# Performance work log

Hardware: AMD Instinct MI355X
Metric: run time of the kernel (lower is better)

Reference implementation:

```python
import jax, jax.numpy as jnp
import numpy as np

N, E, D, ED, G = 100000, 1600000, 64, 64, 512  # nodes, edges, node_dim, edge_dim, graphs
LN_EPS = 1e-5


def setup_inputs() -> dict:
    key = jax.random.key(0)
    ks = jax.random.split(key, 16)
    s_e = 1.0 / np.sqrt(ED)
    s_n = 1.0 / np.sqrt(D)
    inp = {
        'x': jax.random.normal(ks[0], (N, D), jnp.float32),
        'edge_index': jax.random.randint(ks[1], (2, E), 0, N, dtype=jnp.int32),
        'edge_attr': jax.random.normal(ks[2], (E, ED), jnp.float32),
        'node2graph': jnp.sort(jax.random.randint(ks[3], (N,), 0, G, dtype=jnp.int32)),
        # conv1 params
        'We1': jax.random.normal(ks[4], (ED, D), jnp.float32) * s_e,
        'be1': jnp.zeros((D,), jnp.float32),
        'Wm1': jax.random.normal(ks[5], (D, D), jnp.float32) * s_n,
        'bm1': jnp.zeros((D,), jnp.float32),
        'eps1': jnp.array([0.1], jnp.float32),
        'gamma1': jnp.ones((D,), jnp.float32),
        'beta1': jnp.zeros((D,), jnp.float32),
        # conv2 params
        'We2': jax.random.normal(ks[6], (ED, D), jnp.float32) * s_e,
        'be2': jnp.zeros((D,), jnp.float32),
        'Wm2': jax.random.normal(ks[7], (D, D), jnp.float32) * s_n,
        'bm2': jnp.zeros((D,), jnp.float32),
        'eps2': jnp.array([0.1], jnp.float32),
        'gamma2': jnp.ones((D,), jnp.float32),
        'beta2': jnp.zeros((D,), jnp.float32),
    }
    return inp


def _gine_conv(x, src, dst, edge_attr, We, be, Wm, bm, eps):
    # message: SiLU(Wm @ relu(x_j + SiLU(We @ e)) )  gathered per edge, scatter-added to dst
    ea = jax.nn.silu(edge_attr @ We + be)                     # (E, D)
    msg = jax.nn.silu(jnp.maximum(x[src] + ea, 0.0) @ Wm + bm)  # (E, D)
    agg = jax.ops.segment_sum(msg, dst, num_segments=x.shape[0])
    return agg + (1.0 + eps) * x


def _graph_norm(x, g, gamma, beta):
    # pyg LayerNorm(mode='graph'): normalize over all nodes*channels per graph
    f = x.shape[1]
    cnt = jax.ops.segment_sum(jnp.ones((x.shape[0],), x.dtype), g, num_segments=G) * f
    cnt = jnp.maximum(cnt, 1.0)
    mean = jax.ops.segment_sum(x.sum(-1), g, num_segments=G) / cnt          # (G,)
    var = jax.ops.segment_sum((x * x).sum(-1), g, num_segments=G) / cnt - mean ** 2
    xn = (x - mean[g][:, None]) / jnp.sqrt(var + LN_EPS)[g][:, None]
    return xn * gamma + beta


def reference(x, edge_index, edge_attr, node2graph,
              We1, be1, Wm1, bm1, eps1, gamma1, beta1,
              We2, be2, Wm2, bm2, eps2, gamma2, beta2):
    src, dst = edge_index[0], edge_index[1]
    identity = x
    # branch 1 (NOTE: the original torch code computes conv1->norm->relu but then
    # overwrites `out` with conv2(x, ...); we reproduce that faithfully)
    out = _gine_conv(x, src, dst, edge_attr, We1, be1, Wm1, bm1, eps1)
    out = _graph_norm(out, node2graph, gamma1, beta1)
    out = jnp.maximum(out, 0.0)
    # branch 2 (takes original x, per source)
    out = _gine_conv(x, src, dst, edge_attr, We2, be2, Wm2, bm2, eps2)
    out = _graph_norm(out, node2graph, gamma2, beta2)
    out = out + identity
    return jnp.maximum(out, 0.0)
```

## Files before the change

### kernel.cpp

```cpp
#include <hip/hip_runtime.h>
#include <math.h>

#define NN 100000
#define NE 1600000
#define NG 512
#define LN_EPS 1e-5f

typedef __attribute__((ext_vector_type(8))) short short8;
typedef __attribute__((ext_vector_type(8))) unsigned short ushort8;
typedef __attribute__((ext_vector_type(4))) float floatx4;

union BF8 { short8 v; short s[8]; };
union U8  { ushort8 v; unsigned short s[8]; };
union F4  { floatx4 v; float f[4]; };

static __device__ __forceinline__ short f2bf(float f) {
    union { float f; unsigned u; } a; a.f = f;
    unsigned u = a.u;
    unsigned r = (u + 0x7fffu + ((u >> 16) & 1u)) >> 16;
    return (short)r;
}
static __device__ __forceinline__ float bf2f(unsigned short h) {
    union { unsigned u; float f; } a; a.u = ((unsigned)h) << 16;
    return a.f;
}
static __device__ __forceinline__ float silu_f(float v) {
    return v / (1.0f + __expf(-v));
}

__global__ __launch_bounds__(256)
void edge_kernel(const float* __restrict__ x,
                 const int* __restrict__ src,
                 const int* __restrict__ dst,
                 const float* __restrict__ eattr,
                 const float* __restrict__ We,
                 const float* __restrict__ be,
                 const float* __restrict__ Wm,
                 const float* __restrict__ bm,
                 float* __restrict__ agg)
{
    __shared__ unsigned short lds[4][16 * 72];
    const int lane = threadIdx.x & 63;
    const int wid  = threadIdx.x >> 6;
    const int m = lane & 15;
    const int q = lane >> 4;
    unsigned short* tile = lds[wid];

    short8 wef[2][4], wmf[2][4];
    float bev[4], bmv[4];
    #pragma unroll
    for (int kh = 0; kh < 2; ++kh) {
        #pragma unroll
        for (int t = 0; t < 4; ++t) {
            BF8 fe, fm;
            #pragma unroll
            for (int j = 0; j < 8; ++j) {
                const int k = kh * 32 + q * 8 + j;
                const int n = m + 16 * t;
                fe.s[j] = f2bf(We[k * 64 + n]);
                fm.s[j] = f2bf(Wm[k * 64 + n]);
            }
            wef[kh][t] = fe.v; wmf[kh][t] = fm.v;
        }
    }
    #pragma unroll
    for (int t = 0; t < 4; ++t) { bev[t] = be[m + 16 * t]; bmv[t] = bm[m + 16 * t]; }

    const int n_tiles = NE / 16;
    const int stride  = gridDim.x * 4;
    for (int tl = blockIdx.x * 4 + wid; tl < n_tiles; tl += stride) {
        const int e0 = tl * 16;

        short8 a1[2];
        #pragma unroll
        for (int kh = 0; kh < 2; ++kh) {
            const float* p = eattr + (size_t)(e0 + m) * 64 + kh * 32 + q * 8;
            F4 v0, v1; v0.v = *(const floatx4*)p; v1.v = *(const floatx4*)(p + 4);
            BF8 f;
            #pragma unroll
            for (int j = 0; j < 4; ++j) { f.s[j] = f2bf(v0.f[j]); f.s[j + 4] = f2bf(v1.f[j]); }
            a1[kh] = f.v;
        }
        floatx4 acc[4];
        #pragma unroll
        for (int t = 0; t < 4; ++t) acc[t] = (floatx4){0.f, 0.f, 0.f, 0.f};
        #pragma unroll
        for (int kh = 0; kh < 2; ++kh)
            #pragma unroll
            for (int t = 0; t < 4; ++t)
                acc[t] = __builtin_amdgcn_mfma_f32_16x16x32_bf16(a1[kh], wef[kh][t], acc[t], 0, 0, 0);

        #pragma unroll
        for (int t = 0; t < 4; ++t)
            #pragma unroll
            for (int r = 0; r < 4; ++r) {
                const float v = silu_f(acc[t][r] + bev[t]);
                tile[(q * 4 + r) * 72 + m + 16 * t] = (unsigned short)f2bf(v);
            }
        __asm__ volatile("s_waitcnt lgkmcnt(0)" ::: "memory");

        const int sn = src[e0 + m];
        short8 a2[2];
        #pragma unroll
        for (int kh = 0; kh < 2; ++kh) {
            U8 t8; t8.v = *(const ushort8*)&tile[m * 72 + kh * 32 + q * 8];
            const float* xp = x + (size_t)sn * 64 + kh * 32 + q * 8;
            F4 x0, x1; x0.v = *(const floatx4*)xp; x1.v = *(const floatx4*)(xp + 4);
            BF8 f;
            #pragma unroll
            for (int j = 0; j < 4; ++j) {
                f.s[j]     = f2bf(fmaxf(bf2f(t8.s[j])     + x0.f[j], 0.0f));
                f.s[j + 4] = f2bf(fmaxf(bf2f(t8.s[j + 4]) + x1.f[j], 0.0f));
            }
            a2[kh] = f.v;
        }
        #pragma unroll
        for (int t = 0; t < 4; ++t) acc[t] = (floatx4){0.f, 0.f, 0.f, 0.f};
        #pragma unroll
        for (int kh = 0; kh < 2; ++kh)
            #pragma unroll
            for (int t = 0; t < 4; ++t)
                acc[t] = __builtin_amdgcn_mfma_f32_16x16x32_bf16(a2[kh], wmf[kh][t], acc[t], 0, 0, 0);

        int dn[4];
        #pragma unroll
        for (int r = 0; r < 4; ++r) dn[r] = dst[e0 + q * 4 + r];
        #pragma unroll
        for (int t = 0; t < 4; ++t)
            #pragma unroll
            for (int r = 0; r < 4; ++r) {
                const float v = silu_f(acc[t][r] + bmv[t]);
                atomicAdd(agg + (size_t)dn[r] * 64 + (m + 16 * t), v);
            }
    }
}

__global__ __launch_bounds__(256)
void stats_kernel(const float* __restrict__ agg,
                  const float* __restrict__ x,
                  const int* __restrict__ n2g,
                  const float* __restrict__ eps,
                  float* __restrict__ gsum,
                  float* __restrict__ gss,
                  float* __restrict__ gcnt)
{
    const int lane = threadIdx.x & 63;
    const int wid  = threadIdx.x >> 6;
    const float k = 1.0f + eps[0];
    const int stride = gridDim.x * 4;
    for (int n = blockIdx.x * 4 + wid; n < NN; n += stride) {
        const float pre = agg[(size_t)n * 64 + lane] + k * x[(size_t)n * 64 + lane];
        float s = pre, ss = pre * pre;
        #pragma unroll
        for (int off = 32; off > 0; off >>= 1) {
            s  += __shfl_down(s, off, 64);
            ss += __shfl_down(ss, off, 64);
        }
        if (lane == 0) {
            const int g = n2g[n];
            atomicAdd(&gsum[g], s);
            atomicAdd(&gss[g], ss);
            atomicAdd(&gcnt[g], 1.0f);
        }
    }
}

__global__ __launch_bounds__(256)
void norm_kernel(const float* __restrict__ x,
                 const int* __restrict__ n2g,
                 const float* __restrict__ eps,
                 const float* __restrict__ gamma,
                 const float* __restrict__ beta,
                 const float* __restrict__ gsum,
                 const float* __restrict__ gss,
                 const float* __restrict__ gcnt,
                 float* __restrict__ out)
{
    const float k = 1.0f + eps[0];
    const int total = NN * 16;
    for (int idx = blockIdx.x * blockDim.x + threadIdx.x; idx < total;
         idx += gridDim.x * blockDim.x) {
        const int n  = idx >> 4;
        const int c4 = (idx & 15) * 4;
        const int g  = n2g[n];
        const float cnt  = fmaxf(gcnt[g] * 64.0f, 1.0f);
        const float mean = gsum[g] / cnt;
        const float var  = gss[g] / cnt - mean * mean;
        const float rsig = rsqrtf(var + LN_EPS);
        F4 a, xv, o;
        a.v  = *(const floatx4*)&out[(size_t)n * 64 + c4];
        xv.v = *(const floatx4*)&x[(size_t)n * 64 + c4];
        #pragma unroll
        for (int j = 0; j < 4; ++j) {
            const float pre = a.f[j] + k * xv.f[j];
            const float v = (pre - mean) * rsig * gamma[c4 + j] + beta[c4 + j] + xv.f[j];
            o.f[j] = fmaxf(v, 0.0f);
        }
        *(floatx4*)&out[(size_t)n * 64 + c4] = o.v;
    }
}

extern "C" void kernel_launch(void* const* d_in, const int* in_sizes, int n_in,
                              void* d_out, int out_size, void* d_ws, size_t ws_size,
                              hipStream_t stream)
{
    const float* x      = (const float*)d_in[0];
    const int*   ei     = (const int*)  d_in[1];
    const float* eattr  = (const float*)d_in[2];
    const int*   n2g    = (const int*)  d_in[3];
    const float* We2    = (const float*)d_in[11];
    const float* be2    = (const float*)d_in[12];
    const float* Wm2    = (const float*)d_in[13];
    const float* bm2    = (const float*)d_in[14];
    const float* eps2   = (const float*)d_in[15];
    const float* gamma2 = (const float*)d_in[16];
    const float* beta2  = (const float*)d_in[17];

    float* out  = (float*)d_out;
    float* gsum = (float*)d_ws;
    float* gss  = gsum + NG;
    float* gcnt = gss + NG;

    hipMemsetAsync(d_out, 0, (size_t)NN * 64 * sizeof(float), stream);
    hipMemsetAsync(d_ws, 0, 3 * NG * sizeof(float), stream);

    edge_kernel<<<dim3(2048), dim3(256), 0, stream>>>(
        x, ei, ei + NE, eattr, We2, be2, Wm2, bm2, out);
    stats_kernel<<<dim3(1024), dim3(256), 0, stream>>>(
        out, x, n2g, eps2, gsum, gss, gcnt);
    norm_kernel<<<dim3(1024), dim3(256), 0, stream>>>(
        x, n2g, eps2, gamma2, beta2, gsum, gss, gcnt, out);
}
```

Before: 1.064 ms.

## Sort edges by destination and combine duplicate atomics; chunk stats reduction per wave

Builds a destination-sorted permutation of the edges on device each call, using a histogram, a three-kernel scan and an atomic scatter. The edge kernel then processes edges in that order and merges runs of equal destinations within each group of four rows before issuing atomics. The stats kernel now gives each wave a contiguous chunk of nodes and accumulates per graph, flushing only when the graph id changes, which cuts its atomic count. The trade-off is several extra kernel launches and random, uncoalesced gathers of edge_attr through the permutation. With average in-degree 16 and random edges, sorted neighbours in a 16-edge tile will often share a destination.

```diff
diff --git a/kernel.cpp b/kernel.cpp
--- a/kernel.cpp
+++ b/kernel.cpp
@@ -29,10 +29,92 @@
 }
 
 __global__ __launch_bounds__(256)
+void hist_kernel(const int* __restrict__ dst, int* __restrict__ cnt)
+{
+    for (int e = blockIdx.x * blockDim.x + threadIdx.x; e < NE;
+         e += gridDim.x * blockDim.x)
+        atomicAdd(&cnt[dst[e]], 1);
+}
+
+#define SCAN_CHUNK 1024
+#define SCAN_NB ((NN + SCAN_CHUNK - 1) / SCAN_CHUNK)
+
+__global__ __launch_bounds__(256)
+void scan_partial_kernel(const int* __restrict__ cnt, int* __restrict__ bsums)
+{
+    __shared__ int sdata[256];
+    const int b = blockIdx.x, t = threadIdx.x;
+    const int base = b * SCAN_CHUNK + t * 4;
+    int s = 0;
+    #pragma unroll
+    for (int i = 0; i < 4; ++i) {
+        const int idx = base + i;
+        s += (idx < NN) ? cnt[idx] : 0;
+    }
+    sdata[t] = s;
+    __syncthreads();
+    for (int off = 128; off > 0; off >>= 1) {
+        if (t < off) sdata[t] += sdata[t + off];
+        __syncthreads();
+    }
+    if (t == 0) bsums[b] = sdata[0];
+}
+
+__global__ void scan_top_kernel(int* __restrict__ bsums)
+{
+    if (threadIdx.x == 0 && blockIdx.x == 0) {
+        int run = 0;
+        for (int i = 0; i < SCAN_NB; ++i) { const int v = bsums[i]; bsums[i] = run; run += v; }
+    }
+}
+
+__global__ __launch_bounds__(256)
+void scan_final_kernel(int* __restrict__ cnt, const int* __restrict__ bsums)
+{
+    __shared__ int sdata[256];
+    const int b = blockIdx.x, t = threadIdx.x;
+    const int base = b * SCAN_CHUNK + t * 4;
+    int c[4];
+    #pragma unroll
+    for (int i = 0; i < 4; ++i) {
+        const int idx = base + i;
+        c[i] = (idx < NN) ? cnt[idx] : 0;
+    }
+    const int tsum = c[0] + c[1] + c[2] + c[3];
+    sdata[t] = tsum;
+    __syncthreads();
+    for (int off = 1; off < 256; off <<= 1) {
+        const int v = (t >= off) ? sdata[t - off] : 0;
+        __syncthreads();
+        sdata[t] += v;
+        __syncthreads();
+    }
+    int off0 = bsums[b] + sdata[t] - tsum;
+    #pragma unroll
+    for (int i = 0; i < 4; ++i) {
+        const int idx = base + i;
+        if (idx < NN) cnt[idx] = off0;
+        off0 += c[i];
+    }
+}
+
+__global__ __launch_bounds__(256)
+void scatter_kernel(const int* __restrict__ dst, int* __restrict__ starts,
+                    int* __restrict__ perm)
+{
+    for (int e = blockIdx.x * blockDim.x + threadIdx.x; e < NE;
+         e += gridDim.x * blockDim.x) {
+        const int pos = atomicAdd(&starts[dst[e]], 1);
+        perm[pos] = e;
+    }
+}
+
+__global__ __launch_bounds__(256)
 void edge_kernel(const float* __restrict__ x,
                  const int* __restrict__ src,
                  const int* __restrict__ dst,
                  const float* __restrict__ eattr,
+                 const int* __restrict__ perm,
                  const float* __restrict__ We,
                  const float* __restrict__ be,
                  const float* __restrict__ Wm,
@@ -70,11 +152,12 @@
     const int stride  = gridDim.x * 4;
     for (int tl = blockIdx.x * 4 + wid; tl < n_tiles; tl += stride) {
         const int e0 = tl * 16;
+        const int em = perm ? perm[e0 + m] : (e0 + m);
 
         short8 a1[2];
         #pragma unroll
         for (int kh = 0; kh < 2; ++kh) {
-            const float* p = eattr + (size_t)(e0 + m) * 64 + kh * 32 + q * 8;
+            const float* p = eattr + (size_t)em * 64 + kh * 32 + q * 8;
             F4 v0, v1; v0.v = *(const floatx4*)p; v1.v = *(const floatx4*)(p + 4);
             BF8 f;
             #pragma unroll
@@ -99,7 +182,7 @@
             }
         __asm__ volatile("s_waitcnt lgkmcnt(0)" ::: "memory");
 
-        const int sn = src[e0 + m];
+        const int sn = src[em];
         short8 a2[2];
         #pragma unroll
         for (int kh = 0; kh < 2; ++kh) {
@@ -124,17 +207,31 @@
 
         int dn[4];
         #pragma unroll
-        for (int r = 0; r < 4; ++r) dn[r] = dst[e0 + q * 4 + r];
+        for (int r = 0; r < 4; ++r) {
+            const int er = perm ? __shfl(em, q * 4 + r, 64) : (e0 + q * 4 + r);
+            dn[r] = dst[er];
+        }
+        float sv[4][4];
         #pragma unroll
         for (int t = 0; t < 4; ++t)
             #pragma unroll
-            for (int r = 0; r < 4; ++r) {
-                const float v = silu_f(acc[t][r] + bmv[t]);
-                atomicAdd(agg + (size_t)dn[r] * 64 + (m + 16 * t), v);
-            }
-    }
-}
-
+            for (int r = 0; r < 4; ++r)
+                sv[t][r] = silu_f(acc[t][r] + bmv[t]);
+        #pragma unroll
+        for (int t = 0; t < 4; ++t) {
+            const int col = m + 16 * t;
+            float run = sv[t][0];
+            #pragma unroll
+            for (int r = 1; r < 4; ++r) {
+                if (dn[r] == dn[r - 1]) run += sv[t][r];
+                else { atomicAdd(agg + (size_t)dn[r - 1] * 64 + col, run); run = sv[t][r]; }
+            }
+            atomicAdd(agg + (size_t)dn[3] * 64 + col, run);
+        }
+    }
+}
+
+#define STATS_WAVES 4096
 __global__ __launch_bounds__(256)
 void stats_kernel(const float* __restrict__ agg,
                   const float* __restrict__ x,
@@ -146,22 +243,44 @@
 {
     const int lane = threadIdx.x & 63;
     const int wid  = threadIdx.x >> 6;
+    const int w    = blockIdx.x * 4 + wid;
+    const int chunk = (NN + STATS_WAVES - 1) / STATS_WAVES;
+    const int n0 = w * chunk;
+    const int n1 = min(NN, n0 + chunk);
+    if (n0 >= n1) return;
     const float k = 1.0f + eps[0];
-    const int stride = gridDim.x * 4;
-    for (int n = blockIdx.x * 4 + wid; n < NN; n += stride) {
+
+    int   curg = n2g[n0];
+    float s = 0.f, ss = 0.f, rc = 0.f;
+    for (int n = n0; n < n1; ++n) {
+        const int g = n2g[n];
+        if (g != curg) {
+            float a = s, b = ss;
+            #pragma unroll
+            for (int off = 32; off > 0; off >>= 1) {
+                a += __shfl_down(a, off, 64);
+                b += __shfl_down(b, off, 64);
+            }
+            if (lane == 0) {
+                atomicAdd(&gsum[curg], a);
+                atomicAdd(&gss[curg], b);
+                atomicAdd(&gcnt[curg], rc);
+            }
+            s = 0.f; ss = 0.f; rc = 0.f; curg = g;
+        }
         const float pre = agg[(size_t)n * 64 + lane] + k * x[(size_t)n * 64 + lane];
-        float s = pre, ss = pre * pre;
-        #pragma unroll
-        for (int off = 32; off > 0; off >>= 1) {
-            s  += __shfl_down(s, off, 64);
-            ss += __shfl_down(ss, off, 64);
-        }
-        if (lane == 0) {
-            const int g = n2g[n];
-            atomicAdd(&gsum[g], s);
-            atomicAdd(&gss[g], ss);
-            atomicAdd(&gcnt[g], 1.0f);
-        }
+        s += pre; ss += pre * pre; rc += (lane == 0) ? 1.0f : 0.0f;
+    }
+    float a = s, b = ss;
+    #pragma unroll
+    for (int off = 32; off > 0; off >>= 1) {
+        a += __shfl_down(a, off, 64);
+        b += __shfl_down(b, off, 64);
+    }
+    if (lane == 0) {
+        atomicAdd(&gsum[curg], a);
+        atomicAdd(&gss[curg], b);
+        atomicAdd(&gcnt[curg], rc);
     }
 }
 
@@ -215,18 +334,35 @@
     const float* eps2   = (const float*)d_in[15];
     const float* gamma2 = (const float*)d_in[16];
     const float* beta2  = (const float*)d_in[17];
+    const int* src = ei;
+    const int* dst = ei + NE;
 
     float* out  = (float*)d_out;
     float* gsum = (float*)d_ws;
     float* gss  = gsum + NG;
     float* gcnt = gss + NG;
+    int*   bsums = (int*)(gcnt + NG);
+    int*   cnt   = bsums + 256;
+    int*   perm  = cnt + NN;
+    const size_t ws_need = (size_t)(3 * NG + 256 + NN + NE) * 4;
+    const bool do_sort = ws_size >= ws_need;
 
     hipMemsetAsync(d_out, 0, (size_t)NN * 64 * sizeof(float), stream);
-    hipMemsetAsync(d_ws, 0, 3 * NG * sizeof(float), stream);
+    if (do_sort) {
+        hipMemsetAsync(d_ws, 0, (size_t)(3 * NG + 256 + NN) * 4, stream);
+        hist_kernel<<<dim3(512), dim3(256), 0, stream>>>(dst, cnt);
+        scan_partial_kernel<<<dim3(SCAN_NB), dim3(256), 0, stream>>>(cnt, bsums);
+        scan_top_kernel<<<dim3(1), dim3(64), 0, stream>>>(bsums);
+        scan_final_kernel<<<dim3(SCAN_NB), dim3(256), 0, stream>>>(cnt, bsums);
+        scatter_kernel<<<dim3(512), dim3(256), 0, stream>>>(dst, cnt, perm);
+    } else {
+        hipMemsetAsync(d_ws, 0, 3 * NG * sizeof(float), stream);
+    }
 
     edge_kernel<<<dim3(2048), dim3(256), 0, stream>>>(
-        x, ei, ei + NE, eattr, We2, be2, Wm2, bm2, out);
-    stats_kernel<<<dim3(1024), dim3(256), 0, stream>>>(
+        x, src, dst, eattr, do_sort ? perm : (const int*)nullptr,
+        We2, be2, Wm2, bm2, out);
+    stats_kernel<<<dim3(STATS_WAVES / 4), dim3(256), 0, stream>>>(
         out, x, n2g, eps2, gsum, gss, gcnt);
     norm_kernel<<<dim3(1024), dim3(256), 0, stream>>>(
         x, n2g, eps2, gamma2, beta2, gsum, gss, gcnt, out);
```

After: 1.105 ms. +3.9%, slower.
